# Kernel optimization log

Measured on AMD Instinct MI355X. Metric: run time of the kernel, lower is better.

## Reference

```python
import jax, jax.numpy as jnp
import numpy as np

IN_FEATURES = 4096
OUT_FEATURES = 4096
ROWS_PER_BLOCK = OUT_FEATURES // 2  # two (d, n) config blocks of rows
D = 2  # codeword dimension for both blocks


def setup_inputs() -> dict:
    key = jax.random.key(0)
    ks = jax.random.split(key, 6)
    x = jax.random.normal(ks[0], (2, 2048, IN_FEATURES), dtype=jnp.float32)
    codes_2_256 = jax.random.randint(ks[1], (ROWS_PER_BLOCK, IN_FEATURES // D), 0, 256, dtype=jnp.int32)
    codes_2_16 = jax.random.randint(ks[2], (ROWS_PER_BLOCK, IN_FEATURES // D), 0, 16, dtype=jnp.int32)
    grid_2_256 = jax.random.normal(ks[3], (256, D), dtype=jnp.float32)
    grid_2_16 = jax.random.normal(ks[4], (16, D), dtype=jnp.float32)
    scales = jax.random.uniform(ks[5], (OUT_FEATURES,), dtype=jnp.float32, minval=0.5, maxval=1.5)
    bias = jax.random.normal(jax.random.fold_in(key, 7), (OUT_FEATURES,), dtype=jnp.float32)
    return {
        "x": x,
        "codes_2_256": codes_2_256,
        "codes_2_16": codes_2_16,
        "grid_2_256": grid_2_256,
        "grid_2_16": grid_2_16,
        "scales": scales,
        "bias": bias,
    }


def _dequant_block(codes, grid, rows):
    # codes: [rows, in/d] int -> grid lookup [rows, in/d, d] -> [rows, in]
    return grid[codes].reshape(rows, IN_FEATURES)


def reference(x, codes_2_256, codes_2_16, grid_2_256, grid_2_16, scales, bias):
    # Reconstruct weight blocks from per-group VQ codebooks (HIGGS dequant).
    w_top = _dequant_block(codes_2_256, grid_2_256, ROWS_PER_BLOCK)    # [2048, 4096]
    w_bot = _dequant_block(codes_2_16, grid_2_16, ROWS_PER_BLOCK)      # [2048, 4096]
    weight = jnp.concatenate([w_top, w_bot], axis=0) * scales[:, None]  # [out, in]
    # y = x @ W^T + b  (F.linear)
    y = jnp.einsum("bsi,oi->bso", x, weight) + bias
    return y
```

## Files before the change

### kernel.cpp

```cpp
#include <hip/hip_runtime.h>
#include <hip/hip_fp16.h>


#define M_TOK 4096
#define K_DIM 4096
#define N_DIM 4096
#define NT    (K_DIM / 64)

typedef _Float16 half8 __attribute__((ext_vector_type(8)));
typedef float floatx4 __attribute__((ext_vector_type(4)));

__global__ void dequant_w(const int* __restrict__ c256, const int* __restrict__ c16,
                          const float* __restrict__ g256, const float* __restrict__ g16,
                          const float* __restrict__ scales,
                          _Float16* __restrict__ Wh)
{
    int idx = blockIdx.x * blockDim.x + threadIdx.x;
    int row = idx >> 9;
    float s = scales[row];
    int4 cd;
    const float* g;
    if (row < 2048) { cd = ((const int4*)c256)[idx]; g = g256; }
    else            { cd = ((const int4*)c16)[idx - (2048*2048/4)]; g = g16; }
    union U { _Float16 h[8]; ulong2 u; } w;
    w.h[0] = (_Float16)(g[2*cd.x]   * s);
    w.h[1] = (_Float16)(g[2*cd.x+1] * s);
    w.h[2] = (_Float16)(g[2*cd.y]   * s);
    w.h[3] = (_Float16)(g[2*cd.y+1] * s);
    w.h[4] = (_Float16)(g[2*cd.z]   * s);
    w.h[5] = (_Float16)(g[2*cd.z+1] * s);
    w.h[6] = (_Float16)(g[2*cd.w]   * s);
    w.h[7] = (_Float16)(g[2*cd.w+1] * s);
    ((ulong2*)Wh)[idx] = w.u;
}

__global__ void cast_x(const float* __restrict__ x, _Float16* __restrict__ xh)
{
    int idx = blockIdx.x * blockDim.x + threadIdx.x;
    float4 v0 = ((const float4*)x)[2*idx];
    float4 v1 = ((const float4*)x)[2*idx + 1];
    union U { _Float16 h[8]; ulong2 u; } o;
    o.h[0] = (_Float16)v0.x; o.h[1] = (_Float16)v0.y;
    o.h[2] = (_Float16)v0.z; o.h[3] = (_Float16)v0.w;
    o.h[4] = (_Float16)v1.x; o.h[5] = (_Float16)v1.y;
    o.h[6] = (_Float16)v1.z; o.h[7] = (_Float16)v1.w;
    ((ulong2*)xh)[idx] = o.u;
}

__device__ __forceinline__ void gl2lds16(const void* g, void* l)
{
    __builtin_amdgcn_global_load_lds(
        (const __attribute__((address_space(1))) void*)g,
        (__attribute__((address_space(3))) void*)l, 16, 0, 0);
}

#define STAGE(buf, unit, pan, kcol)                                          \
    { _Float16* lb = &lds[(buf)*32768 + (unit)*8192];                        \
      gl2lds16((pan) + goff0 + (kcol), lb + t*8);                            \
      gl2lds16((pan) + goff1 + (kcol), lb + (512+t)*8); }

#define RD_A(q, mm) (*(const half8*)&lds[cur*32768 + ((q)>>1)*2*8192 +       \
      ((wr*8 + ((q)&1)*4 + (mm))*64 + kbr*16 + lrow)*8])
#define RD_B(q, n)  (*(const half8*)&lds[cur*32768 + (((q)>>1)*2+1)*8192 +   \
      ((wc*4 + (n))*64 + kbr*16 + lrow)*8])

#define PHASE_MFMA(q)                                                        \
    __builtin_amdgcn_s_setprio(1);                                           \
    _Pragma("unroll")                                                        \
    for (int mm = 0; mm < 4; ++mm) {                                         \
        _Pragma("unroll")                                                    \
        for (int n = 0; n < 4; ++n)                                          \
            acc[((q)&1)*4+mm][n] = __builtin_amdgcn_mfma_f32_16x16x32_f16(   \
                a[mm], b[n], acc[((q)&1)*4+mm][n], 0, 0, 0);                 \
    }                                                                        \
    __builtin_amdgcn_s_setprio(0);

#define BOUNDARY(morev)                                                      \
    if (morev) asm volatile("s_waitcnt vmcnt(4)" ::: "memory");              \
    else       asm volatile("s_waitcnt vmcnt(0)" ::: "memory");              \
    __builtin_amdgcn_s_barrier();                                            \
    asm volatile("" ::: "memory");

__global__ __launch_bounds__(512, 2)
void gemm8p(const _Float16* __restrict__ Xh, const _Float16* __restrict__ Wh,
            const float* __restrict__ bias, float* __restrict__ C)
{
    extern __shared__ _Float16 lds[];

    const int t    = threadIdx.x;
    const int lane = t & 63;
    const int w    = t >> 6;
    const int wr   = w >> 2;
    const int wc   = w & 3;
    const int lrow = lane & 15;
    const int kbr  = lane >> 4;

    const int swz  = (blockIdx.x & 7) * 32 + (blockIdx.x >> 3);
    const int bx   = swz & 15;
    const int by   = swz >> 4;
    const int brow = by * 256;
    const int bcol = bx * 256;

    const int idx0 = t,        idx1 = 512 + t;
    const size_t goff0 = (size_t)((idx0 >> 6)*16 + (idx0 & 15)) * K_DIM + ((idx0 >> 4) & 3)*8;
    const size_t goff1 = (size_t)((idx1 >> 6)*16 + (idx1 & 15)) * K_DIM + ((idx1 >> 4) & 3)*8;

    const _Float16* Apan = Xh + (size_t)brow * K_DIM;
    const _Float16* Bpan = Wh + (size_t)bcol * K_DIM;

    floatx4 acc[8][4];
    #pragma unroll
    for (int m = 0; m < 8; ++m)
        #pragma unroll
        for (int n = 0; n < 4; ++n)
            #pragma unroll
            for (int r = 0; r < 4; ++r) acc[m][n][r] = 0.0f;

    STAGE(0, 0, Apan, 0);
    STAGE(0, 1, Bpan, 0);
    STAGE(0, 2, Apan, 32);
    STAGE(0, 3, Bpan, 32);

    for (int tau = 0; tau < NT; ++tau) {
        const int  cur  = tau & 1;
        const int  nxt  = cur ^ 1;
        const int  kn   = (tau + 1) * 64;
        const bool more = (tau + 1 < NT);
        half8 a[4], b[4];

        BOUNDARY(more);
        #pragma unroll
        for (int n = 0; n < 4; ++n)  b[n] = RD_B(0, n);
        #pragma unroll
        for (int mm = 0; mm < 4; ++mm) a[mm] = RD_A(0, mm);
        if (more) STAGE(nxt, 0, Apan, kn);
        PHASE_MFMA(0);

        #pragma unroll
        for (int mm = 0; mm < 4; ++mm) a[mm] = RD_A(1, mm);
        if (more) STAGE(nxt, 1, Bpan, kn);
        PHASE_MFMA(1);

        BOUNDARY(more);
        #pragma unroll
        for (int n = 0; n < 4; ++n)  b[n] = RD_B(2, n);
        #pragma unroll
        for (int mm = 0; mm < 4; ++mm) a[mm] = RD_A(2, mm);
        if (more) STAGE(nxt, 2, Apan, kn + 32);
        PHASE_MFMA(2);

        #pragma unroll
        for (int mm = 0; mm < 4; ++mm) a[mm] = RD_A(3, mm);
        if (more) STAGE(nxt, 3, Bpan, kn + 32);
        PHASE_MFMA(3);
    }

    #pragma unroll
    for (int n = 0; n < 4; ++n) {
        const int col = bcol + wc*64 + n*16 + lrow;
        const float bv = bias[col];
        #pragma unroll
        for (int m = 0; m < 8; ++m) {
            const int rbase = brow + wr*128 + m*16 + kbr*4;
            #pragma unroll
            for (int r = 0; r < 4; ++r)
                C[(size_t)(rbase + r) * N_DIM + col] = acc[m][n][r] + bv;
        }
    }
}

extern "C" void kernel_launch(void* const* d_in, const int* in_sizes, int n_in,
                              void* d_out, int out_size, void* d_ws, size_t ws_size,
                              hipStream_t stream)
{
    const float* x      = (const float*)d_in[0];
    const int*   c256   = (const int*)  d_in[1];
    const int*   c16    = (const int*)  d_in[2];
    const float* g256   = (const float*)d_in[3];
    const float* g16    = (const float*)d_in[4];
    const float* scales = (const float*)d_in[5];
    const float* bias   = (const float*)d_in[6];
    float*       out    = (float*)d_out;

    char* ws = (char*)d_ws;
    const size_t SZ = (size_t)K_DIM * N_DIM * sizeof(_Float16);
    _Float16* Wh = (_Float16*)(ws + 0*SZ);
    _Float16* Xh = (_Float16*)(ws + 1*SZ);

    hipFuncSetAttribute((const void*)gemm8p,
                        hipFuncAttributeMaxDynamicSharedMemorySize, 131072);

    dequant_w<<<dim3((4096*2048/4)/256), dim3(256), 0, stream>>>(
        c256, c16, g256, g16, scales, Wh);
    cast_x<<<dim3((M_TOK*K_DIM/8)/256), dim3(256), 0, stream>>>(x, Xh);
    gemm8p<<<dim3(256), dim3(512), 131072, stream>>>(Xh, Wh, bias, out);
}
```

Measured before the change: 295.3 us.

## Restructure GEMM main loop to one barrier per K-tile with explicit LDS waits

Reworks the GEMM main loop so all four global-to-LDS stages for the next K-tile are issued at the start of each iteration. The two mid-iteration vmcnt-plus-barrier boundaries are replaced by a single vmcnt(0) and barrier at the end of the iteration. LDS fragment reads for all four phases go into separate registers, and explicit lgkmcnt waits plus sched_barriers let MFMAs start as soon as their operands arrive while later reads are still in flight. The intent is to cut barrier stalls and overlap LDS latency with MFMA work. The cost is more VGPRs for the extra fragment buffers and a coarser wait on the global prefetch.

```diff
diff --git a/kernel.cpp b/kernel.cpp
--- a/kernel.cpp
+++ b/kernel.cpp
@@ -64,22 +64,23 @@
 #define RD_B(q, n)  (*(const half8*)&lds[cur*32768 + (((q)>>1)*2+1)*8192 +   \
       ((wc*4 + (n))*64 + kbr*16 + lrow)*8])
 
-#define PHASE_MFMA(q)                                                        \
+#define SB0() __builtin_amdgcn_sched_barrier(0)
+
+#define LGKM(n)                                                              \
+    asm volatile("s_waitcnt lgkmcnt(" #n ")" ::: "memory");                  \
+    __builtin_amdgcn_sched_barrier(0);
+
+#define MFMA_CL(row, areg, breg)                                             \
     __builtin_amdgcn_s_setprio(1);                                           \
     _Pragma("unroll")                                                        \
     for (int mm = 0; mm < 4; ++mm) {                                         \
         _Pragma("unroll")                                                    \
         for (int n = 0; n < 4; ++n)                                          \
-            acc[((q)&1)*4+mm][n] = __builtin_amdgcn_mfma_f32_16x16x32_f16(   \
-                a[mm], b[n], acc[((q)&1)*4+mm][n], 0, 0, 0);                 \
+            acc[(row)*4+mm][n] = __builtin_amdgcn_mfma_f32_16x16x32_f16(     \
+                areg[mm], breg[n], acc[(row)*4+mm][n], 0, 0, 0);             \
     }                                                                        \
-    __builtin_amdgcn_s_setprio(0);
-
-#define BOUNDARY(morev)                                                      \
-    if (morev) asm volatile("s_waitcnt vmcnt(4)" ::: "memory");              \
-    else       asm volatile("s_waitcnt vmcnt(0)" ::: "memory");              \
-    __builtin_amdgcn_s_barrier();                                            \
-    asm volatile("" ::: "memory");
+    __builtin_amdgcn_s_setprio(0);                                           \
+    __builtin_amdgcn_sched_barrier(0);
 
 __global__ __launch_bounds__(512, 2)
 void gemm8p(const _Float16* __restrict__ Xh, const _Float16* __restrict__ Wh,
@@ -120,39 +121,49 @@
     STAGE(0, 1, Bpan, 0);
     STAGE(0, 2, Apan, 32);
     STAGE(0, 3, Bpan, 32);
+    asm volatile("s_waitcnt vmcnt(0)" ::: "memory");
+    __builtin_amdgcn_s_barrier();
 
     for (int tau = 0; tau < NT; ++tau) {
         const int  cur  = tau & 1;
         const int  nxt  = cur ^ 1;
         const int  kn   = (tau + 1) * 64;
         const bool more = (tau + 1 < NT);
-        half8 a[4], b[4];
-
-        BOUNDARY(more);
-        #pragma unroll
-        for (int n = 0; n < 4; ++n)  b[n] = RD_B(0, n);
-        #pragma unroll
-        for (int mm = 0; mm < 4; ++mm) a[mm] = RD_A(0, mm);
-        if (more) STAGE(nxt, 0, Apan, kn);
-        PHASE_MFMA(0);
-
-        #pragma unroll
-        for (int mm = 0; mm < 4; ++mm) a[mm] = RD_A(1, mm);
-        if (more) STAGE(nxt, 1, Bpan, kn);
-        PHASE_MFMA(1);
-
-        BOUNDARY(more);
-        #pragma unroll
-        for (int n = 0; n < 4; ++n)  b[n] = RD_B(2, n);
-        #pragma unroll
-        for (int mm = 0; mm < 4; ++mm) a[mm] = RD_A(2, mm);
-        if (more) STAGE(nxt, 2, Apan, kn + 32);
-        PHASE_MFMA(2);
-
-        #pragma unroll
-        for (int mm = 0; mm < 4; ++mm) a[mm] = RD_A(3, mm);
-        if (more) STAGE(nxt, 3, Bpan, kn + 32);
-        PHASE_MFMA(3);
+        half8 a0[4], a1[4], a2[4], a3[4], b01[4], b23[4];
+
+        #pragma unroll
+        for (int n = 0; n < 4; ++n)  b01[n] = RD_B(0, n);
+        #pragma unroll
+        for (int mm = 0; mm < 4; ++mm) a0[mm] = RD_A(0, mm);
+        SB0();
+        #pragma unroll
+        for (int mm = 0; mm < 4; ++mm) a1[mm] = RD_A(1, mm);
+        if (more) {
+            STAGE(nxt, 0, Apan, kn);
+            STAGE(nxt, 1, Bpan, kn);
+            STAGE(nxt, 2, Apan, kn + 32);
+            STAGE(nxt, 3, Bpan, kn + 32);
+        }
+        LGKM(4);
+        MFMA_CL(0, a0, b01);
+
+        #pragma unroll
+        for (int n = 0; n < 4; ++n)  b23[n] = RD_B(2, n);
+        #pragma unroll
+        for (int mm = 0; mm < 4; ++mm) a2[mm] = RD_A(2, mm);
+        LGKM(8);
+        MFMA_CL(1, a1, b01);
+
+        #pragma unroll
+        for (int mm = 0; mm < 4; ++mm) a3[mm] = RD_A(3, mm);
+        LGKM(4);
+        MFMA_CL(0, a2, b23);
+
+        LGKM(0);
+        MFMA_CL(1, a3, b23);
+
+        asm volatile("s_waitcnt vmcnt(0)" ::: "memory");
+        __builtin_amdgcn_s_barrier();
     }
 
     #pragma unroll
```

Result: slower. 313.3 us (+6.1%).
